# Kernel tuning notes

Measured on AMD Instinct MI355X. Metric: run time of the kernel, lower is better.

Reference implementation:

```python
import jax, jax.numpy as jnp
import numpy as np

N_USER = 100_000
N_ITEM = 100_000
E = 1_600_000
D_IN = 128
H = 64
OUT = 2


def _lin_init(k, din, dout):
    kw, kb = jax.random.split(k)
    bound = 1.0 / np.sqrt(din)
    W = jax.random.uniform(kw, (din, dout), jnp.float32, -bound, bound)
    b = jax.random.uniform(kb, (dout,), jnp.float32, -bound, bound)
    return W, b


def setup_inputs() -> dict:
    key = jax.random.key(0)
    ks = jax.random.split(key, 12)
    inp = {
        "x_user": jax.random.normal(ks[0], (N_USER, D_IN), jnp.float32),
        "x_item": jax.random.normal(ks[1], (N_ITEM, D_IN), jnp.float32),
        "ei_user": jax.random.randint(ks[2], (2, E), 0, N_USER, jnp.int32),
        "ei_item": jax.random.randint(ks[3], (2, E), 0, N_ITEM, jnp.int32),
    }
    inp["W1_user"], inp["b1_user"] = _lin_init(ks[4], D_IN, H)
    inp["W1_item"], inp["b1_item"] = _lin_init(ks[5], D_IN, H)
    inp["W2_user"], inp["b2_user"] = _lin_init(ks[6], H, H)
    inp["W2_item"], inp["b2_item"] = _lin_init(ks[7], H, H)
    inp["Wl_user"], inp["bl_user"] = _lin_init(ks[8], H, OUT)
    inp["Wl_item"], inp["bl_item"] = _lin_init(ks[9], H, OUT)
    return inp


def gcn_conv(x, W, b, src, dst, n):
    # PyG GCNConv: h = x @ W; symmetric norm with added self-loops; scatter-add to dst; + bias
    loop = jnp.arange(n, dtype=src.dtype)
    s = jnp.concatenate([src, loop])  # [E+n]
    d = jnp.concatenate([dst, loop])
    deg = jax.ops.segment_sum(jnp.ones(s.shape[0], x.dtype), d, num_segments=n)
    dinv = jnp.where(deg > 0, jax.lax.rsqrt(deg), 0.0)
    norm = dinv[s] * dinv[d]  # [E+n]
    h = x @ W  # [n, out]
    msg = h[s] * norm[:, None]  # gather + scale, [E+n, out]
    return jax.ops.segment_sum(msg, d, num_segments=n) + b


def reference(x_user, x_item, ei_user, ei_item,
              W1_user, b1_user, W1_item, b1_item,
              W2_user, b2_user, W2_item, b2_item,
              Wl_user, bl_user, Wl_item, bl_item):
    # layer 1 (HeteroConv with one GCNConv per node type's relation) + relu; dropout = identity (eval)
    h_u = jax.nn.relu(gcn_conv(x_user, W1_user, b1_user, ei_user[0], ei_user[1], N_USER))
    h_i = jax.nn.relu(gcn_conv(x_item, W1_item, b1_item, ei_item[0], ei_item[1], N_ITEM))
    # layer 2 + relu
    h_u = jax.nn.relu(gcn_conv(h_u, W2_user, b2_user, ei_user[0], ei_user[1], N_USER))
    h_i = jax.nn.relu(gcn_conv(h_i, W2_item, b2_item, ei_item[0], ei_item[1], N_ITEM))
    # per-node-type output heads
    return (h_u @ Wl_user + bl_user, h_i @ Wl_item + bl_item)
```

## Files before the change

### kernel.cpp

```cpp
#include <hip/hip_runtime.h>

#define CDIV(a,b) (((a)+(b)-1)/(b))
#define NPB 256
#define PCHUNK 2048

typedef __attribute__((ext_vector_type(8))) short bf16x8;
typedef __attribute__((ext_vector_type(8))) unsigned short u16x8;
typedef __attribute__((ext_vector_type(4))) float f32x4;

__device__ __forceinline__ unsigned short f2bf(float x){
    unsigned int u = __float_as_uint(x);
    unsigned int r = u + 0x7FFFu + ((u >> 16) & 1u);
    return (unsigned short)(r >> 16);
}
__device__ __forceinline__ float bf2f(unsigned short h){
    return __uint_as_float(((unsigned int)h) << 16);
}

__global__ __launch_bounds__(256) void hg_wsplit_all(const float* __restrict__ W1u, const float* __restrict__ W1i,
                                                     const float* __restrict__ W2u, const float* __restrict__ W2i,
                                                     unsigned short* __restrict__ Bhi, unsigned short* __restrict__ Blo){
    const int sid = blockIdx.x*256 + threadIdx.x;
    if (sid >= 3072) return;
    const float* W; int slot, base;
    if (sid < 1024)      { W = W1u; slot = sid;        base = 0;     }
    else if (sid < 2048) { W = W1i; slot = sid - 1024; base = 8192;  }
    else if (sid < 2560) { W = W2u; slot = sid - 2048; base = 16384; }
    else                 { W = W2i; slot = sid - 2560; base = 20480; }
    const int l  = slot & 63;
    const int ct = (slot >> 6) & 3;
    const int ks = slot >> 8;
    const int kb = ks*32 + (l >> 4)*8;
    const int c  = ct*16 + (l & 15);
    #pragma unroll
    for (int j = 0; j < 8; ++j){
        const float w = W[(size_t)(kb + j)*64 + c];
        const unsigned short h = f2bf(w);
        Bhi[(size_t)base + (size_t)slot*8 + j] = h;
        Blo[(size_t)base + (size_t)slot*8 + j] = f2bf(w - bf2f(h));
    }
}

__device__ __forceinline__ void gemm1_body(int gb,
                                           const float* __restrict__ XU, const float* __restrict__ XI,
                                           const unsigned short* __restrict__ Bhi, const unsigned short* __restrict__ Blo,
                                           unsigned short* __restrict__ GU, unsigned short* __restrict__ GI,
                                           int NU, int NI, int gbU){
    const int type = (gb >= gbU);
    const int blk  = type ? gb - gbU : gb;
    const float* X = type ? XI : XU;
    unsigned short* G = type ? GI : GU;
    const int N    = type ? NI : NU;
    const unsigned short* Bh = Bhi + (type ? 8192 : 0);
    const unsigned short* Bl = Blo + (type ? 8192 : 0);

    const int l = threadIdx.x & 63;
    const int w = threadIdx.x >> 6;
    const int row0 = blk*64 + w*16;
    if (row0 >= N) return;

    f32x4 acc[4];
    #pragma unroll
    for (int ct = 0; ct < 4; ++ct) acc[ct] = (f32x4){0.f,0.f,0.f,0.f};

    const int rA = row0 + (l & 15);
    const int kg = (l >> 4) * 8;
    const bool rowok = (rA < N);
    const float* xrow = X + (size_t)rA * 128;

    #pragma unroll
    for (int ks = 0; ks < 4; ++ks){
        float xv[8];
        if (rowok){
            const float4 a = *(const float4*)(xrow + ks*32 + kg);
            const float4 b = *(const float4*)(xrow + ks*32 + kg + 4);
            xv[0]=a.x; xv[1]=a.y; xv[2]=a.z; xv[3]=a.w;
            xv[4]=b.x; xv[5]=b.y; xv[6]=b.z; xv[7]=b.w;
        } else {
            #pragma unroll
            for (int j = 0; j < 8; ++j) xv[j] = 0.f;
        }
        bf16x8 ahi, alo;
        #pragma unroll
        for (int j = 0; j < 8; ++j){
            const unsigned short h = f2bf(xv[j]);
            ahi[j] = (short)h;
            alo[j] = (short)f2bf(xv[j] - bf2f(h));
        }
        #pragma unroll
        for (int ct = 0; ct < 4; ++ct){
            const bf16x8 bhi = *(const bf16x8*)(Bh + ((size_t)(ks*4 + ct)*64 + l)*8);
            const bf16x8 blo = *(const bf16x8*)(Bl + ((size_t)(ks*4 + ct)*64 + l)*8);
            acc[ct] = __builtin_amdgcn_mfma_f32_16x16x32_bf16(ahi, bhi, acc[ct], 0, 0, 0);
            acc[ct] = __builtin_amdgcn_mfma_f32_16x16x32_bf16(alo, bhi, acc[ct], 0, 0, 0);
            acc[ct] = __builtin_amdgcn_mfma_f32_16x16x32_bf16(ahi, blo, acc[ct], 0, 0, 0);
        }
    }

    const int orow0 = row0 + (l >> 4)*4;
    const int ocol  = l & 15;
    #pragma unroll
    for (int r = 0; r < 4; ++r){
        const int orow = orow0 + r;
        if (orow < N){
            #pragma unroll
            for (int ct = 0; ct < 4; ++ct)
                G[(size_t)orow*64 + ct*16 + ocol] = f2bf(acc[ct][r]);
        }
    }
}

#define GEMM_TAIL(taskTot) \
    if ((int)blockIdx.x >= (taskTot)){ \
        gemm1_body(goff + blockIdx.x - (taskTot), XU, XI, Bhi, Blo, GU, GI, NU, NI, gbU); \
        return; \
    }

__global__ __launch_bounds__(256) void hg_mega_chist(const int* __restrict__ eiU, const int* __restrict__ eiI,
                                                     int* __restrict__ chU, int* __restrict__ chI,
                                                     int EU, int EI, int pbU, int pbTot, int NB,
                                                     const float* __restrict__ XU, const float* __restrict__ XI,
                                                     const unsigned short* __restrict__ Bhi, const unsigned short* __restrict__ Blo,
                                                     unsigned short* __restrict__ GU, unsigned short* __restrict__ GI,
                                                     int NU, int NI, int gbU, int goff){
    GEMM_TAIL(pbTot)
    extern __shared__ int sh[];
    const int type = ((int)blockIdx.x >= pbU);
    const int blk  = type ? blockIdx.x - pbU : blockIdx.x;
    const int E    = type ? EI : EU;
    const int* dst = (type ? eiI : eiU) + E;
    int* chist     = (type ? chI : chU) + (size_t)blk * NB;
    for (int i = threadIdx.x; i < NB; i += 256) sh[i] = 0;
    __syncthreads();
    const int e0 = blk * PCHUNK;
    const int eend = min(e0 + PCHUNK, E);
    for (int e = e0 + threadIdx.x; e < eend; e += 256)
        atomicAdd(&sh[dst[e] >> 8], 1);
    __syncthreads();
    for (int i = threadIdx.x; i < NB; i += 256)
        chist[i] = sh[i];
}

__global__ __launch_bounds__(256) void hg_mega_colscan(int* __restrict__ chU, int* __restrict__ chI,
                                                       int* __restrict__ bhU, int* __restrict__ bhI,
                                                       int pbU, int pbI, int NB,
                                                       const float* __restrict__ XU, const float* __restrict__ XI,
                                                       const unsigned short* __restrict__ Bhi, const unsigned short* __restrict__ Blo,
                                                       unsigned short* __restrict__ GU, unsigned short* __restrict__ GI,
                                                       int NU, int NI, int gbU, int goff){
    GEMM_TAIL(2*NB)
    __shared__ int sc[256];
    const int type = ((int)blockIdx.x >= NB);
    const int b    = type ? blockIdx.x - NB : blockIdx.x;
    int* chist     = type ? chI : chU;
    int* bh        = type ? bhI : bhU;
    const int nch  = type ? pbI : pbU;
    const int t = threadIdx.x;
    int carry = 0;
    for (int seg = 0; seg < nch; seg += 256){
        const int idx = seg + t;
        const int v = (idx < nch) ? chist[(size_t)idx*NB + b] : 0;
        sc[t] = v;
        __syncthreads();
        for (int off = 1; off < 256; off <<= 1){
            int x = 0;
            if (t >= off) x = sc[t-off];
            __syncthreads();
            if (t >= off) sc[t] += x;
            __syncthreads();
        }
        if (idx < nch) chist[(size_t)idx*NB + b] = carry + sc[t] - v;
        const int tot = sc[255];
        __syncthreads();
        carry += tot;
    }
    if (t == 0) bh[b] = carry;
}

__global__ __launch_bounds__(256) void hg_mega_bscan(const int* __restrict__ bhU, const int* __restrict__ bhI,
                                                     int* __restrict__ boffU, int* __restrict__ boffI,
                                                     int NB, int EU, int EI,
                                                     const float* __restrict__ XU, const float* __restrict__ XI,
                                                     const unsigned short* __restrict__ Bhi, const unsigned short* __restrict__ Blo,
                                                     unsigned short* __restrict__ GU, unsigned short* __restrict__ GI,
                                                     int NU, int NI, int gbU, int goff){
    GEMM_TAIL(2)
    __shared__ int sc[256];
    const int type = blockIdx.x;
    const int* bh = type ? bhI : bhU;
    int* boff     = type ? boffI : boffU;
    const int E   = type ? EI : EU;
    const int t = threadIdx.x;
    const int i0 = 2*t, i1 = 2*t + 1;
    const int c0 = (i0 < NB) ? bh[i0] : 0;
    const int c1 = (i1 < NB) ? bh[i1] : 0;
    const int s = c0 + c1;
    sc[t] = s;
    __syncthreads();
    for (int off = 1; off < 256; off <<= 1){
        int x = 0;
        if (t >= off) x = sc[t-off];
        __syncthreads();
        if (t >= off) sc[t] += x;
        __syncthreads();
    }
    const int excl = sc[t] - s;
    if (i0 < NB) boff[i0] = excl;
    if (i1 < NB) boff[i1] = excl + c0;
    if (t == 0) boff[NB] = E;
}

__global__ __launch_bounds__(256) void hg_mega_part(const int* __restrict__ eiU, const int* __restrict__ eiI,
                                                    const int* __restrict__ chU, const int* __restrict__ chI,
                                                    const int* __restrict__ boffU, const int* __restrict__ boffI,
                                                    unsigned int* __restrict__ bkU, unsigned int* __restrict__ bkI,
                                                    int EU, int EI, int pbU, int pbTot, int NB,
                                                    const float* __restrict__ XU, const float* __restrict__ XI,
                                                    const unsigned short* __restrict__ Bhi, const unsigned short* __restrict__ Blo,
                                                    unsigned short* __restrict__ GU, unsigned short* __restrict__ GI,
                                                    int NU, int NI, int gbU, int goff){
    GEMM_TAIL(pbTot)
    extern __shared__ int sh[];
    int* lofs  = sh;
    int* lcur  = lofs + NB;
    int* lbase = lcur + NB;
    int* sc    = lbase + NB;
    unsigned int* stage = (unsigned int*)(sc + 256);
    int* gaddr = (int*)(stage + PCHUNK);

    const int type = ((int)blockIdx.x >= pbU);
    const int blk  = type ? blockIdx.x - pbU : blockIdx.x;
    const int E    = type ? EI : EU;
    const int* src = type ? eiI : eiU;
    const int* dst = src + E;
    const int* chist = (type ? chI : chU) + (size_t)blk * NB;
    const int* boff  = type ? boffI : boffU;
    unsigned int* bucketed = type ? bkI : bkU;

    const int t  = threadIdx.x;
    const int e0 = blk * PCHUNK;
    const int eend = min(e0 + PCHUNK, E);
    const int cnt  = eend - e0;

    int se[8], de[8];
    for (int i = t; i < NB; i += 256) lofs[i] = 0;
    __syncthreads();
    const int eb = e0 + t*8;
    if (eb + 8 <= E){
        const int4 sa = *(const int4*)(src + eb);
        const int4 sb = *(const int4*)(src + eb + 4);
        const int4 da = *(const int4*)(dst + eb);
        const int4 db = *(const int4*)(dst + eb + 4);
        se[0]=sa.x; se[1]=sa.y; se[2]=sa.z; se[3]=sa.w;
        se[4]=sb.x; se[5]=sb.y; se[6]=sb.z; se[7]=sb.w;
        de[0]=da.x; de[1]=da.y; de[2]=da.z; de[3]=da.w;
        de[4]=db.x; de[5]=db.y; de[6]=db.z; de[7]=db.w;
    } else {
        #pragma unroll
        for (int j = 0; j < 8; ++j){
            const int e = eb + j;
            se[j] = (e < E) ? src[e] : -1;
            de[j] = (e < E) ? dst[e] : -1;
        }
    }
    #pragma unroll
    for (int j = 0; j < 8; ++j)
        if (de[j] >= 0) atomicAdd(&lofs[de[j] >> 8], 1);
    __syncthreads();

    const int i0 = 2*t, i1 = 2*t + 1;
    const int c0 = (i0 < NB) ? lofs[i0] : 0;
    const int c1 = (i1 < NB) ? lofs[i1] : 0;
    if (i0 < NB) lbase[i0] = boff[i0] + chist[i0];
    if (i1 < NB) lbase[i1] = boff[i1] + chist[i1];
    const int s = c0 + c1;
    sc[t] = s;
    __syncthreads();
    for (int off = 1; off < 256; off <<= 1){
        int x = 0;
        if (t >= off) x = sc[t-off];
        __syncthreads();
        if (t >= off) sc[t] += x;
        __syncthreads();
    }
    const int excl = sc[t] - s;
    __syncthreads();
    if (i0 < NB){ lofs[i0] = excl;      lcur[i0] = excl; }
    if (i1 < NB){ lofs[i1] = excl + c0; lcur[i1] = excl + c0; }
    __syncthreads();

    #pragma unroll
    for (int j = 0; j < 8; ++j){
        if (de[j] >= 0){
            const int b = de[j] >> 8;
            const int p = atomicAdd(&lcur[b], 1);
            stage[p] = (unsigned int)se[j] | ((unsigned int)(de[j] & 255) << 24);
            gaddr[p] = lbase[b] + (p - lofs[b]);
        }
    }
    __syncthreads();

    for (int i = t; i < cnt; i += 256)
        bucketed[gaddr[i]] = stage[i];
}

__global__ __launch_bounds__(256) void hg_mega_build(const unsigned int* __restrict__ bkU, const unsigned int* __restrict__ bkI,
                                                     const int* __restrict__ boffU, const int* __restrict__ boffI,
                                                     float* __restrict__ dinvU, float* __restrict__ dinvI,
                                                     int* __restrict__ rowptrU, int* __restrict__ rowptrI,
                                                     int* __restrict__ csrU, int* __restrict__ csrI,
                                                     int NU, int NI, int EU, int EI, int nbU, int nbTot,
                                                     const float* __restrict__ XU, const float* __restrict__ XI,
                                                     const unsigned short* __restrict__ Bhi, const unsigned short* __restrict__ Blo,
                                                     unsigned short* __restrict__ GU, unsigned short* __restrict__ GI,
                                                     int gbU, int goff){
    GEMM_TAIL(nbTot)
    __shared__ int hist[NPB];
    __shared__ int sc[NPB];
    __shared__ int cur[NPB];
    const int type = ((int)blockIdx.x >= nbU);
    const int b    = type ? blockIdx.x - nbU : blockIdx.x;
    const unsigned int* bucketed = type ? bkI : bkU;
    const int* boff = type ? boffI : boffU;
    float* dinv     = type ? dinvI : dinvU;
    int* rowptr     = type ? rowptrI : rowptrU;
    int* csr_src    = type ? csrI : csrU;
    const int N     = type ? NI : NU;
    const int E     = type ? EI : EU;

    const int t   = threadIdx.x;
    const int beg = boff[b], end = boff[b+1];
    hist[t] = 0;
    __syncthreads();
    for (int i = beg + t; i < end; i += 256)
        atomicAdd(&hist[bucketed[i] >> 24], 1);
    __syncthreads();
    const int d = hist[t];
    sc[t] = d;
    __syncthreads();
    for (int off = 1; off < 256; off <<= 1){
        int x = 0;
        if (t >= off) x = sc[t-off];
        __syncthreads();
        if (t >= off) sc[t] += x;
        __syncthreads();
    }
    const int excl = sc[t] - d;
    const int v = b*NPB + t;
    if (v < N){
        dinv[v]   = rsqrtf((float)(d + 1));
        rowptr[v] = beg + excl;
    }
    if (b == 0 && t == 0) rowptr[N] = E;
    cur[t] = beg + excl;
    __syncthreads();
    for (int i = beg + t; i < end; i += 256){
        const unsigned int w = bucketed[i];
        const int p = atomicAdd(&cur[w >> 24], 1);
        csr_src[p] = (int)(w & 0x00FFFFFFu);
    }
}

__device__ __forceinline__ void gather_core(const unsigned short* __restrict__ g,
                                            const int* __restrict__ csr_src, const int* __restrict__ rowptr,
                                            const float* __restrict__ dinv, int v, int c8, bool ok,
                                            float* acc, float& dvv){
    int beg = 0, cnt = 0;
    dvv = 0.f;
    if (ok){ beg = rowptr[v]; cnt = rowptr[v+1] - beg; dvv = dinv[v]; }

    #pragma unroll
    for (int j = 0; j < 8; ++j) acc[j] = 0.f;
    if (ok){
        const u16x8 s = *(const u16x8*)(g + (size_t)v*64 + c8);
        #pragma unroll
        for (int j = 0; j < 8; ++j) acc[j] = bf2f(s[j]) * dvv;
    }

    int i = 0;
    for (; i + 8 <= cnt; i += 8){
        const int s0 = csr_src[beg+i+0]; const int s1 = csr_src[beg+i+1];
        const int s2 = csr_src[beg+i+2]; const int s3 = csr_src[beg+i+3];
        const int s4 = csr_src[beg+i+4]; const int s5 = csr_src[beg+i+5];
        const int s6 = csr_src[beg+i+6]; const int s7 = csr_src[beg+i+7];
        const float dv0 = dinv[s0]; const float dv1 = dinv[s1];
        const float dv2 = dinv[s2]; const float dv3 = dinv[s3];
        const float dv4 = dinv[s4]; const float dv5 = dinv[s5];
        const float dv6 = dinv[s6]; const float dv7 = dinv[s7];
        const u16x8 x0 = *(const u16x8*)(g + (size_t)s0*64 + c8);
        const u16x8 x1 = *(const u16x8*)(g + (size_t)s1*64 + c8);
        const u16x8 x2 = *(const u16x8*)(g + (size_t)s2*64 + c8);
        const u16x8 x3 = *(const u16x8*)(g + (size_t)s3*64 + c8);
        const u16x8 x4 = *(const u16x8*)(g + (size_t)s4*64 + c8);
        const u16x8 x5 = *(const u16x8*)(g + (size_t)s5*64 + c8);
        const u16x8 x6 = *(const u16x8*)(g + (size_t)s6*64 + c8);
        const u16x8 x7 = *(const u16x8*)(g + (size_t)s7*64 + c8);
        #pragma unroll
        for (int j = 0; j < 8; ++j){
            float a = fmaf(bf2f(x0[j]), dv0, fmaf(bf2f(x1[j]), dv1, fmaf(bf2f(x2[j]), dv2, bf2f(x3[j]) * dv3)));
            float c = fmaf(bf2f(x4[j]), dv4, fmaf(bf2f(x5[j]), dv5, fmaf(bf2f(x6[j]), dv6, bf2f(x7[j]) * dv7)));
            acc[j] += a + c;
        }
    }
    for (; i + 4 <= cnt; i += 4){
        const int s0 = csr_src[beg+i+0]; const int s1 = csr_src[beg+i+1];
        const int s2 = csr_src[beg+i+2]; const int s3 = csr_src[beg+i+3];
        const float dv0 = dinv[s0]; const float dv1 = dinv[s1];
        const float dv2 = dinv[s2]; const float dv3 = dinv[s3];
        const u16x8 x0 = *(const u16x8*)(g + (size_t)s0*64 + c8);
        const u16x8 x1 = *(const u16x8*)(g + (size_t)s1*64 + c8);
        const u16x8 x2 = *(const u16x8*)(g + (size_t)s2*64 + c8);
        const u16x8 x3 = *(const u16x8*)(g + (size_t)s3*64 + c8);
        #pragma unroll
        for (int j = 0; j < 8; ++j)
            acc[j] += fmaf(bf2f(x0[j]), dv0, fmaf(bf2f(x1[j]), dv1, fmaf(bf2f(x2[j]), dv2, bf2f(x3[j]) * dv3)));
    }
    for (; i < cnt; ++i){
        const int s0 = csr_src[beg+i];
        const float dv0 = dinv[s0];
        const u16x8 x0 = *(const u16x8*)(g + (size_t)s0*64 + c8);
        #pragma unroll
        for (int j = 0; j < 8; ++j) acc[j] = fmaf(bf2f(x0[j]), dv0, acc[j]);
    }
}

__global__ __launch_bounds__(256) void hg_agg_gemm2(const unsigned short* __restrict__ gU, const unsigned short* __restrict__ gI,
                                                    const int* __restrict__ csrU, const int* __restrict__ csrI,
                                                    const int* __restrict__ rowptrU, const int* __restrict__ rowptrI,
                                                    const float* __restrict__ dinvU, const float* __restrict__ dinvI,
                                                    const float* __restrict__ bU, const float* __restrict__ bI,
                                                    const unsigned short* __restrict__ Bhi, const unsigned short* __restrict__ Blo,
                                                    unsigned short* __restrict__ G2U, unsigned short* __restrict__ G2I,
                                                    int NU, int NI, int nbU){
    __shared__ float hrow[32*68];
    const int type = ((int)blockIdx.x >= nbU);
    const int blk  = type ? blockIdx.x - nbU : blockIdx.x;
    const unsigned short* g = type ? gI : gU;
    const int* csr_src = type ? csrI : csrU;
    const int* rowptr  = type ? rowptrI : rowptrU;
    const float* dinv  = type ? dinvI : dinvU;
    const float* b     = type ? bI : bU;
    unsigned short* G2 = type ? G2I : G2U;
    const int N        = type ? NI : NU;
    const unsigned short* Bh = Bhi + (type ? 20480 : 16384);
    const unsigned short* Bl = Blo + (type ? 20480 : 16384);

    const int t = threadIdx.x;
    const int nodeLocal = t >> 3;
    const int c8 = (t & 7) << 3;
    const int v = blk*32 + nodeLocal;
    const bool ok = (v < N);

    float acc[8]; float dvv;
    gather_core(g, csr_src, rowptr, dinv, v, c8, ok, acc, dvv);

    {
        const float4 b0 = *(const float4*)(b + c8);
        const float4 b1 = *(const float4*)(b + c8 + 4);
        float r0 = ok ? fmaxf(fmaf(acc[0], dvv, b0.x), 0.f) : 0.f;
        float r1 = ok ? fmaxf(fmaf(acc[1], dvv, b0.y), 0.f) : 0.f;
        float r2 = ok ? fmaxf(fmaf(acc[2], dvv, b0.z), 0.f) : 0.f;
        float r3 = ok ? fmaxf(fmaf(acc[3], dvv, b0.w), 0.f) : 0.f;
        float r4 = ok ? fmaxf(fmaf(acc[4], dvv, b1.x), 0.f) : 0.f;
        float r5 = ok ? fmaxf(fmaf(acc[5], dvv, b1.y), 0.f) : 0.f;
        float r6 = ok ? fmaxf(fmaf(acc[6], dvv, b1.z), 0.f) : 0.f;
        float r7 = ok ? fmaxf(fmaf(acc[7], dvv, b1.w), 0.f) : 0.f;
        float* hr = hrow + nodeLocal*68 + c8;
        hr[0]=r0; hr[1]=r1; hr[2]=r2; hr[3]=r3; hr[4]=r4; hr[5]=r5; hr[6]=r6; hr[7]=r7;
    }
    __syncthreads();

    const int l  = t & 63;
    const int wv = t >> 6;
    const int rbase  = (wv & 1) * 16;
    const int ctbase = (wv >> 1) * 2;

    f32x4 acc2[2];
    acc2[0] = (f32x4){0.f,0.f,0.f,0.f};
    acc2[1] = (f32x4){0.f,0.f,0.f,0.f};

    const int arow = rbase + (l & 15);
    const int kg   = (l >> 4) * 8;
    #pragma unroll
    for (int ks = 0; ks < 2; ++ks){
        const float* hr = hrow + arow*68 + ks*32 + kg;
        const float4 a = *(const float4*)(hr);
        const float4 c = *(const float4*)(hr + 4);
        float xv[8] = {a.x,a.y,a.z,a.w,c.x,c.y,c.z,c.w};
        bf16x8 ahi, alo;
        #pragma unroll
        for (int j = 0; j < 8; ++j){
            const unsigned short h = f2bf(xv[j]);
            ahi[j] = (short)h;
            alo[j] = (short)f2bf(xv[j] - bf2f(h));
        }
        #pragma unroll
        for (int ct = 0; ct < 2; ++ct){
            const int slot = (ks*4 + ctbase + ct)*64 + l;
            const bf16x8 bhi = *(const bf16x8*)(Bh + (size_t)slot*8);
            const bf16x8 blo = *(const bf16x8*)(Bl + (size_t)slot*8);
            acc2[ct] = __builtin_amdgcn_mfma_f32_16x16x32_bf16(ahi, bhi, acc2[ct], 0, 0, 0);
            acc2[ct] = __builtin_amdgcn_mfma_f32_16x16x32_bf16(alo, bhi, acc2[ct], 0, 0, 0);
            acc2[ct] = __builtin_amdgcn_mfma_f32_16x16x32_bf16(ahi, blo, acc2[ct], 0, 0, 0);
        }
    }

    const int orow0 = rbase + (l >> 4)*4;
    const int ocol  = l & 15;
    #pragma unroll
    for (int r = 0; r < 4; ++r){
        const int gv = blk*32 + orow0 + r;
        if (gv < N){
            #pragma unroll
            for (int ct = 0; ct < 2; ++ct)
                G2[(size_t)gv*64 + (ctbase + ct)*16 + ocol] = f2bf(acc2[ct][r]);
        }
    }
}

__global__ __launch_bounds__(256) void hg_agghead(const unsigned short* __restrict__ gU, const unsigned short* __restrict__ gI,
                                                  const int* __restrict__ csrU, const int* __restrict__ csrI,
                                                  const int* __restrict__ rowptrU, const int* __restrict__ rowptrI,
                                                  const float* __restrict__ dinvU, const float* __restrict__ dinvI,
                                                  const float* __restrict__ bU, const float* __restrict__ bI,
                                                  const float* __restrict__ WlU, const float* __restrict__ WlI,
                                                  const float* __restrict__ blU, const float* __restrict__ blI,
                                                  float* __restrict__ outU, float* __restrict__ outI,
                                                  int NU, int NI, int nbU){
    const int type = ((int)blockIdx.x >= nbU);
    const int blk  = type ? blockIdx.x - nbU : blockIdx.x;
    const unsigned short* g = type ? gI : gU;
    const int* csr_src = type ? csrI : csrU;
    const int* rowptr  = type ? rowptrI : rowptrU;
    const float* dinv  = type ? dinvI : dinvU;
    const float* b     = type ? bI : bU;
    const float* Wl    = type ? WlI : WlU;
    const float* bl    = type ? blI : blU;
    float* outp        = type ? outI : outU;
    const int N        = type ? NI : NU;

    const int t = threadIdx.x;
    const int nodeLocal = t >> 3;
    const int c8 = (t & 7) << 3;
    const int v = blk*32 + nodeLocal;
    const bool ok = (v < N);

    float acc[8]; float dvv;
    gather_core(g, csr_src, rowptr, dinv, v, c8, ok, acc, dvv);

    float r[8];
    {
        const float4 b0 = *(const float4*)(b + c8);
        const float4 b1 = *(const float4*)(b + c8 + 4);
        r[0] = fmaxf(fmaf(acc[0], dvv, b0.x), 0.f);
        r[1] = fmaxf(fmaf(acc[1], dvv, b0.y), 0.f);
        r[2] = fmaxf(fmaf(acc[2], dvv, b0.z), 0.f);
        r[3] = fmaxf(fmaf(acc[3], dvv, b0.w), 0.f);
        r[4] = fmaxf(fmaf(acc[4], dvv, b1.x), 0.f);
        r[5] = fmaxf(fmaf(acc[5], dvv, b1.y), 0.f);
        r[6] = fmaxf(fmaf(acc[6], dvv, b1.z), 0.f);
        r[7] = fmaxf(fmaf(acc[7], dvv, b1.w), 0.f);
    }

    float p0 = 0.f, p1 = 0.f;
    #pragma unroll
    for (int j = 0; j < 8; ++j){
        const float2 wl = *(const float2*)(Wl + (size_t)(c8 + j)*2);
        p0 = fmaf(r[j], wl.x, p0);
        p1 = fmaf(r[j], wl.y, p1);
    }
    p0 += __shfl_xor(p0, 1); p1 += __shfl_xor(p1, 1);
    p0 += __shfl_xor(p0, 2); p1 += __shfl_xor(p1, 2);
    p0 += __shfl_xor(p0, 4); p1 += __shfl_xor(p1, 4);
    if (ok && (t & 7) == 0){
        float2 o; o.x = p0 + bl[0]; o.y = p1 + bl[1];
        *(float2*)(outp + (size_t)v*2) = o;
    }
}

extern "C" void kernel_launch(void* const* d_in, const int* in_sizes, int n_in,
                              void* d_out, int out_size, void* d_ws, size_t ws_size,
                              hipStream_t stream) {
    const float* x_user = (const float*)d_in[0];
    const float* x_item = (const float*)d_in[1];
    const int*  ei_user = (const int*)d_in[2];
    const int*  ei_item = (const int*)d_in[3];
    const float* W1_user = (const float*)d_in[4];
    const float* b1_user = (const float*)d_in[5];
    const float* W1_item = (const float*)d_in[6];
    const float* b1_item = (const float*)d_in[7];
    const float* W2_user = (const float*)d_in[8];
    const float* b2_user = (const float*)d_in[9];
    const float* W2_item = (const float*)d_in[10];
    const float* b2_item = (const float*)d_in[11];
    const float* Wl_user = (const float*)d_in[12];
    const float* bl_user = (const float*)d_in[13];
    const float* Wl_item = (const float*)d_in[14];
    const float* bl_item = (const float*)d_in[15];

    const int NU = in_sizes[0] / 128;
    const int NI = in_sizes[1] / 128;
    const int EU = in_sizes[2] / 2;
    const int EI = in_sizes[3] / 2;
    const int NBU = CDIV(NU, NPB);
    const int NBI = CDIV(NI, NPB);
    const int NB  = (NBU > NBI) ? NBU : NBI;
    const int pbU = CDIV(EU, PCHUNK), pbI = CDIV(EI, PCHUNK);

    char* w = (char*)d_ws;
    unsigned short* GU = (unsigned short*)w;    w += (size_t)NU * 64 * sizeof(unsigned short);
    unsigned short* GI = (unsigned short*)w;    w += (size_t)NI * 64 * sizeof(unsigned short);
    unsigned short* G2U = (unsigned short*)w;   w += (size_t)NU * 64 * sizeof(unsigned short);
    unsigned short* G2I = (unsigned short*)w;   w += (size_t)NI * 64 * sizeof(unsigned short);
    float* dinvU = (float*)w;                   w += (size_t)NU * sizeof(float);
    float* dinvI = (float*)w;                   w += (size_t)NI * sizeof(float);
    int* rowptrU = (int*)w;                     w += ((size_t)NU + 1) * sizeof(int);
    int* rowptrI = (int*)w;                     w += ((size_t)NI + 1) * sizeof(int);
    int* csrU = (int*)w;                        w += (size_t)EU * sizeof(int);
    int* csrI = (int*)w;                        w += (size_t)EI * sizeof(int);
    unsigned int* bkU = (unsigned int*)w;       w += (size_t)EU * sizeof(int);
    unsigned int* bkI = (unsigned int*)w;       w += (size_t)EI * sizeof(int);
    int* chU = (int*)w;                         w += (size_t)pbU * NB * sizeof(int);
    int* chI = (int*)w;                         w += (size_t)pbI * NB * sizeof(int);
    int* bhU = (int*)w;                         w += (size_t)NB * sizeof(int);
    int* bhI = (int*)w;                         w += (size_t)NB * sizeof(int);
    int* boffU = (int*)w;                       w += ((size_t)NB + 1) * sizeof(int);
    int* boffI = (int*)w;                       w += ((size_t)NB + 1) * sizeof(int);
    unsigned short* Bhi = (unsigned short*)w;   w += (size_t)24576 * sizeof(unsigned short);
    unsigned short* Blo = (unsigned short*)w;   w += (size_t)24576 * sizeof(unsigned short);

    float* out  = (float*)d_out;
    float* outU = out;
    float* outI = out + (size_t)2 * NU;

    const int gbU = CDIV(NU, 64), gbI = CDIV(NI, 64);
    const int GB = gbU + gbI;
    const int q = GB / 5;
    const int c1 = q, c2 = q, c3 = q, c4 = q, c5 = GB - 4*q;

    hg_wsplit_all<<<12, 256, 0, stream>>>(W1_user, W1_item, W2_user, W2_item, Bhi, Blo);

    hg_mega_chist<<<pbU + pbI + c1, 256, NB*sizeof(int), stream>>>(
        ei_user, ei_item, chU, chI, EU, EI, pbU, pbU + pbI, NB,
        x_user, x_item, Bhi, Blo, GU, GI, NU, NI, gbU, 0);
    hg_mega_colscan<<<2*NB + c2, 256, 0, stream>>>(
        chU, chI, bhU, bhI, pbU, pbI, NB,
        x_user, x_item, Bhi, Blo, GU, GI, NU, NI, gbU, c1);
    hg_mega_bscan<<<2 + c3, 256, 0, stream>>>(
        bhU, bhI, boffU, boffI, NB, EU, EI,
        x_user, x_item, Bhi, Blo, GU, GI, NU, NI, gbU, c1 + c2);
    const size_t p5lds = (size_t)(3*NB + 256 + 2*PCHUNK) * sizeof(int);
    hg_mega_part<<<pbU + pbI + c4, 256, p5lds, stream>>>(
        ei_user, ei_item, chU, chI, boffU, boffI, bkU, bkI, EU, EI, pbU, pbU + pbI, NB,
        x_user, x_item, Bhi, Blo, GU, GI, NU, NI, gbU, c1 + c2 + c3);
    hg_mega_build<<<NBU + NBI + c5, 256, 0, stream>>>(
        bkU, bkI, boffU, boffI, dinvU, dinvI, rowptrU, rowptrI, csrU, csrI,
        NU, NI, EU, EI, NBU, NBU + NBI,
        x_user, x_item, Bhi, Blo, GU, GI, gbU, c1 + c2 + c3 + c4);

    const int abU = CDIV(NU, 32), abI = CDIV(NI, 32);
    hg_agg_gemm2<<<abU + abI, 256, 0, stream>>>(GU, GI, csrU, csrI, rowptrU, rowptrI,
                                                dinvU, dinvI, b1_user, b1_item,
                                                Bhi, Blo, G2U, G2I, NU, NI, abU);

    hg_agghead<<<abU + abI, 256, 0, stream>>>(G2U, G2I, csrU, csrI, rowptrU, rowptrI,
                                              dinvU, dinvI, b2_user, b2_item,
                                              Wl_user, Wl_item, bl_user, bl_item,
                                              outU, outI, NU, NI, abU);
}
```

Baseline: 240.7 us.

## Merge weight split into histogram kernel and fold bucket scan via last-block

Cuts the preprocessing chain from six launches to four. The weight bf16 hi/lo split now runs as extra blocks of the histogram kernel. The bucket-offset scan is done by whichever column-scan block finishes last, detected with an atomic counter and threadfence. The layer-1 GEMM tail blocks are spread over three kernels instead of five, and the weight split no longer overlaps with the GEMM because it now shares a kernel with the histogram. The last-block pattern leaves one block doing a serial tail scan, and it relies on the counter being reset inside the first kernel.

```diff
diff --git a/kernel.cpp b/kernel.cpp
--- a/kernel.cpp
+++ b/kernel.cpp
@@ -3,6 +3,7 @@
 #define CDIV(a,b) (((a)+(b)-1)/(b))
 #define NPB 256
 #define PCHUNK 2048
+#define WSB 12
 
 typedef __attribute__((ext_vector_type(8))) short bf16x8;
 typedef __attribute__((ext_vector_type(8))) unsigned short u16x8;
@@ -15,30 +16,6 @@
 }
 __device__ __forceinline__ float bf2f(unsigned short h){
     return __uint_as_float(((unsigned int)h) << 16);
-}
-
-__global__ __launch_bounds__(256) void hg_wsplit_all(const float* __restrict__ W1u, const float* __restrict__ W1i,
-                                                     const float* __restrict__ W2u, const float* __restrict__ W2i,
-                                                     unsigned short* __restrict__ Bhi, unsigned short* __restrict__ Blo){
-    const int sid = blockIdx.x*256 + threadIdx.x;
-    if (sid >= 3072) return;
-    const float* W; int slot, base;
-    if (sid < 1024)      { W = W1u; slot = sid;        base = 0;     }
-    else if (sid < 2048) { W = W1i; slot = sid - 1024; base = 8192;  }
-    else if (sid < 2560) { W = W2u; slot = sid - 2048; base = 16384; }
-    else                 { W = W2i; slot = sid - 2560; base = 20480; }
-    const int l  = slot & 63;
-    const int ct = (slot >> 6) & 3;
-    const int ks = slot >> 8;
-    const int kb = ks*32 + (l >> 4)*8;
-    const int c  = ct*16 + (l & 15);
-    #pragma unroll
-    for (int j = 0; j < 8; ++j){
-        const float w = W[(size_t)(kb + j)*64 + c];
-        const unsigned short h = f2bf(w);
-        Bhi[(size_t)base + (size_t)slot*8 + j] = h;
-        Blo[(size_t)base + (size_t)slot*8 + j] = f2bf(w - bf2f(h));
-    }
 }
 
 __device__ __forceinline__ void gemm1_body(int gb,
@@ -116,17 +93,39 @@
         return; \
     }
 
-__global__ __launch_bounds__(256) void hg_mega_chist(const int* __restrict__ eiU, const int* __restrict__ eiI,
-                                                     int* __restrict__ chU, int* __restrict__ chI,
-                                                     int EU, int EI, int pbU, int pbTot, int NB,
-                                                     const float* __restrict__ XU, const float* __restrict__ XI,
-                                                     const unsigned short* __restrict__ Bhi, const unsigned short* __restrict__ Blo,
-                                                     unsigned short* __restrict__ GU, unsigned short* __restrict__ GI,
-                                                     int NU, int NI, int gbU, int goff){
-    GEMM_TAIL(pbTot)
+__global__ __launch_bounds__(256) void hg_link1(const float* __restrict__ W1u, const float* __restrict__ W1i,
+                                                const float* __restrict__ W2u, const float* __restrict__ W2i,
+                                                unsigned short* __restrict__ Bhi, unsigned short* __restrict__ Blo,
+                                                const int* __restrict__ eiU, const int* __restrict__ eiI,
+                                                int* __restrict__ chU, int* __restrict__ chI,
+                                                int EU, int EI, int pbU, int NB, int* __restrict__ done){
+    if (blockIdx.x == 0 && threadIdx.x == 0) *done = 0;
+    if ((int)blockIdx.x < WSB){
+        const int sid = blockIdx.x*256 + threadIdx.x;
+        if (sid >= 3072) return;
+        const float* W; int slot, base;
+        if (sid < 1024)      { W = W1u; slot = sid;        base = 0;     }
+        else if (sid < 2048) { W = W1i; slot = sid - 1024; base = 8192;  }
+        else if (sid < 2560) { W = W2u; slot = sid - 2048; base = 16384; }
+        else                 { W = W2i; slot = sid - 2560; base = 20480; }
+        const int l  = slot & 63;
+        const int ct = (slot >> 6) & 3;
+        const int ks = slot >> 8;
+        const int kb = ks*32 + (l >> 4)*8;
+        const int c  = ct*16 + (l & 15);
+        #pragma unroll
+        for (int j = 0; j < 8; ++j){
+            const float w = W[(size_t)(kb + j)*64 + c];
+            const unsigned short h = f2bf(w);
+            Bhi[(size_t)base + (size_t)slot*8 + j] = h;
+            Blo[(size_t)base + (size_t)slot*8 + j] = f2bf(w - bf2f(h));
+        }
+        return;
+    }
     extern __shared__ int sh[];
-    const int type = ((int)blockIdx.x >= pbU);
-    const int blk  = type ? blockIdx.x - pbU : blockIdx.x;
+    const int cb   = blockIdx.x - WSB;
+    const int type = (cb >= pbU);
+    const int blk  = type ? cb - pbU : cb;
     const int E    = type ? EI : EU;
     const int* dst = (type ? eiI : eiU) + E;
     int* chist     = (type ? chI : chU) + (size_t)blk * NB;
@@ -141,15 +140,18 @@
         chist[i] = sh[i];
 }
 
-__global__ __launch_bounds__(256) void hg_mega_colscan(int* __restrict__ chU, int* __restrict__ chI,
-                                                       int* __restrict__ bhU, int* __restrict__ bhI,
-                                                       int pbU, int pbI, int NB,
-                                                       const float* __restrict__ XU, const float* __restrict__ XI,
-                                                       const unsigned short* __restrict__ Bhi, const unsigned short* __restrict__ Blo,
-                                                       unsigned short* __restrict__ GU, unsigned short* __restrict__ GI,
-                                                       int NU, int NI, int gbU, int goff){
+__global__ __launch_bounds__(256) void hg_link2(int* __restrict__ chU, int* __restrict__ chI,
+                                                int* __restrict__ bhU, int* __restrict__ bhI,
+                                                int* __restrict__ boffU, int* __restrict__ boffI,
+                                                int pbU, int pbI, int NB, int EU, int EI,
+                                                int* __restrict__ done,
+                                                const float* __restrict__ XU, const float* __restrict__ XI,
+                                                const unsigned short* __restrict__ Bhi, const unsigned short* __restrict__ Blo,
+                                                unsigned short* __restrict__ GU, unsigned short* __restrict__ GI,
+                                                int NU, int NI, int gbU, int goff){
     GEMM_TAIL(2*NB)
     __shared__ int sc[256];
+    __shared__ int winner;
     const int type = ((int)blockIdx.x >= NB);
     const int b    = type ? blockIdx.x - NB : blockIdx.x;
     int* chist     = type ? chI : chU;
@@ -175,50 +177,48 @@
         carry += tot;
     }
     if (t == 0) bh[b] = carry;
-}
-
-__global__ __launch_bounds__(256) void hg_mega_bscan(const int* __restrict__ bhU, const int* __restrict__ bhI,
-                                                     int* __restrict__ boffU, int* __restrict__ boffI,
-                                                     int NB, int EU, int EI,
-                                                     const float* __restrict__ XU, const float* __restrict__ XI,
-                                                     const unsigned short* __restrict__ Bhi, const unsigned short* __restrict__ Blo,
-                                                     unsigned short* __restrict__ GU, unsigned short* __restrict__ GI,
-                                                     int NU, int NI, int gbU, int goff){
-    GEMM_TAIL(2)
-    __shared__ int sc[256];
-    const int type = blockIdx.x;
-    const int* bh = type ? bhI : bhU;
-    int* boff     = type ? boffI : boffU;
-    const int E   = type ? EI : EU;
-    const int t = threadIdx.x;
-    const int i0 = 2*t, i1 = 2*t + 1;
-    const int c0 = (i0 < NB) ? bh[i0] : 0;
-    const int c1 = (i1 < NB) ? bh[i1] : 0;
-    const int s = c0 + c1;
-    sc[t] = s;
-    __syncthreads();
-    for (int off = 1; off < 256; off <<= 1){
-        int x = 0;
-        if (t >= off) x = sc[t-off];
-        __syncthreads();
-        if (t >= off) sc[t] += x;
-        __syncthreads();
-    }
-    const int excl = sc[t] - s;
-    if (i0 < NB) boff[i0] = excl;
-    if (i1 < NB) boff[i1] = excl + c0;
-    if (t == 0) boff[NB] = E;
-}
-
-__global__ __launch_bounds__(256) void hg_mega_part(const int* __restrict__ eiU, const int* __restrict__ eiI,
-                                                    const int* __restrict__ chU, const int* __restrict__ chI,
-                                                    const int* __restrict__ boffU, const int* __restrict__ boffI,
-                                                    unsigned int* __restrict__ bkU, unsigned int* __restrict__ bkI,
-                                                    int EU, int EI, int pbU, int pbTot, int NB,
-                                                    const float* __restrict__ XU, const float* __restrict__ XI,
-                                                    const unsigned short* __restrict__ Bhi, const unsigned short* __restrict__ Blo,
-                                                    unsigned short* __restrict__ GU, unsigned short* __restrict__ GI,
-                                                    int NU, int NI, int gbU, int goff){
+    __threadfence();
+    if (t == 0){
+        const int old = atomicAdd(done, 1);
+        winner = (old == 2*NB - 1);
+    }
+    __syncthreads();
+    if (!winner) return;
+    __threadfence();
+    for (int ty = 0; ty < 2; ++ty){
+        const int* bhp = ty ? bhI : bhU;
+        int* boff      = ty ? boffI : boffU;
+        const int E    = ty ? EI : EU;
+        const int i0 = 2*t, i1 = 2*t + 1;
+        const int c0 = (i0 < NB) ? bhp[i0] : 0;
+        const int c1 = (i1 < NB) ? bhp[i1] : 0;
+        const int s = c0 + c1;
+        sc[t] = s;
+        __syncthreads();
+        for (int off = 1; off < 256; off <<= 1){
+            int x = 0;
+            if (t >= off) x = sc[t-off];
+            __syncthreads();
+            if (t >= off) sc[t] += x;
+            __syncthreads();
+        }
+        const int excl = sc[t] - s;
+        if (i0 < NB) boff[i0] = excl;
+        if (i1 < NB) boff[i1] = excl + c0;
+        if (t == 0) boff[NB] = E;
+        __syncthreads();
+    }
+}
+
+__global__ __launch_bounds__(256) void hg_link3(const int* __restrict__ eiU, const int* __restrict__ eiI,
+                                                const int* __restrict__ chU, const int* __restrict__ chI,
+                                                const int* __restrict__ boffU, const int* __restrict__ boffI,
+                                                unsigned int* __restrict__ bkU, unsigned int* __restrict__ bkI,
+                                                int EU, int EI, int pbU, int pbTot, int NB,
+                                                const float* __restrict__ XU, const float* __restrict__ XI,
+                                                const unsigned short* __restrict__ Bhi, const unsigned short* __restrict__ Blo,
+                                                unsigned short* __restrict__ GU, unsigned short* __restrict__ GI,
+                                                int NU, int NI, int gbU, int goff){
     GEMM_TAIL(pbTot)
     extern __shared__ int sh[];
     int* lofs  = sh;
@@ -304,16 +304,16 @@
         bucketed[gaddr[i]] = stage[i];
 }
 
-__global__ __launch_bounds__(256) void hg_mega_build(const unsigned int* __restrict__ bkU, const unsigned int* __restrict__ bkI,
-                                                     const int* __restrict__ boffU, const int* __restrict__ boffI,
-                                                     float* __restrict__ dinvU, float* __restrict__ dinvI,
-                                                     int* __restrict__ rowptrU, int* __restrict__ rowptrI,
-                                                     int* __restrict__ csrU, int* __restrict__ csrI,
-                                                     int NU, int NI, int EU, int EI, int nbU, int nbTot,
-                                                     const float* __restrict__ XU, const float* __restrict__ XI,
-                                                     const unsigned short* __restrict__ Bhi, const unsigned short* __restrict__ Blo,
-                                                     unsigned short* __restrict__ GU, unsigned short* __restrict__ GI,
-                                                     int gbU, int goff){
+__global__ __launch_bounds__(256) void hg_link4(const unsigned int* __restrict__ bkU, const unsigned int* __restrict__ bkI,
+                                                const int* __restrict__ boffU, const int* __restrict__ boffI,
+                                                float* __restrict__ dinvU, float* __restrict__ dinvI,
+                                                int* __restrict__ rowptrU, int* __restrict__ rowptrI,
+                                                int* __restrict__ csrU, int* __restrict__ csrI,
+                                                int NU, int NI, int EU, int EI, int nbU, int nbTot,
+                                                const float* __restrict__ XU, const float* __restrict__ XI,
+                                                const unsigned short* __restrict__ Bhi, const unsigned short* __restrict__ Blo,
+                                                unsigned short* __restrict__ GU, unsigned short* __restrict__ GI,
+                                                int gbU, int goff){
     GEMM_TAIL(nbTot)
     __shared__ int hist[NPB];
     __shared__ int sc[NPB];
@@ -626,6 +626,7 @@
     int* bhI = (int*)w;                         w += (size_t)NB * sizeof(int);
     int* boffU = (int*)w;                       w += ((size_t)NB + 1) * sizeof(int);
     int* boffI = (int*)w;                       w += ((size_t)NB + 1) * sizeof(int);
+    int* done  = (int*)w;                       w += sizeof(int);
     unsigned short* Bhi = (unsigned short*)w;   w += (size_t)24576 * sizeof(unsigned short);
     unsigned short* Blo = (unsigned short*)w;   w += (size_t)24576 * sizeof(unsigned short);
 
@@ -635,28 +636,26 @@
 
     const int gbU = CDIV(NU, 64), gbI = CDIV(NI, 64);
     const int GB = gbU + gbI;
-    const int q = GB / 5;
-    const int c1 = q, c2 = q, c3 = q, c4 = q, c5 = GB - 4*q;
-
-    hg_wsplit_all<<<12, 256, 0, stream>>>(W1_user, W1_item, W2_user, W2_item, Bhi, Blo);
-
-    hg_mega_chist<<<pbU + pbI + c1, 256, NB*sizeof(int), stream>>>(
-        ei_user, ei_item, chU, chI, EU, EI, pbU, pbU + pbI, NB,
+    const int q = GB / 3;
+    const int c2 = q, c3 = q, c4 = GB - 2*q;
+
+    hg_link1<<<WSB + pbU + pbI, 256, NB*sizeof(int), stream>>>(
+        W1_user, W1_item, W2_user, W2_item, Bhi, Blo,
+        ei_user, ei_item, chU, chI, EU, EI, pbU, NB, done);
+
+    hg_link2<<<2*NB + c2, 256, 0, stream>>>(
+        chU, chI, bhU, bhI, boffU, boffI, pbU, pbI, NB, EU, EI, done,
         x_user, x_item, Bhi, Blo, GU, GI, NU, NI, gbU, 0);
-    hg_mega_colscan<<<2*NB + c2, 256, 0, stream>>>(
-        chU, chI, bhU, bhI, pbU, pbI, NB,
-        x_user, x_item, Bhi, Blo, GU, GI, NU, NI, gbU, c1);
-    hg_mega_bscan<<<2 + c3, 256, 0, stream>>>(
-        bhU, bhI, boffU, boffI, NB, EU, EI,
-        x_user, x_item, Bhi, Blo, GU, GI, NU, NI, gbU, c1 + c2);
+
     const size_t p5lds = (size_t)(3*NB + 256 + 2*PCHUNK) * sizeof(int);
-    hg_mega_part<<<pbU + pbI + c4, 256, p5lds, stream>>>(
+    hg_link3<<<pbU + pbI + c3, 256, p5lds, stream>>>(
         ei_user, ei_item, chU, chI, boffU, boffI, bkU, bkI, EU, EI, pbU, pbU + pbI, NB,
-        x_user, x_item, Bhi, Blo, GU, GI, NU, NI, gbU, c1 + c2 + c3);
-    hg_mega_build<<<NBU + NBI + c5, 256, 0, stream>>>(
+        x_user, x_item, Bhi, Blo, GU, GI, NU, NI, gbU, c2);
+
+    hg_link4<<<NBU + NBI + c4, 256, 0, stream>>>(
         bkU, bkI, boffU, boffI, dinvU, dinvI, rowptrU, rowptrI, csrU, csrI,
         NU, NI, EU, EI, NBU, NBU + NBI,
-        x_user, x_item, Bhi, Blo, GU, GI, gbU, c1 + c2 + c3 + c4);
+        x_user, x_item, Bhi, Blo, GU, GI, gbU, c2 + c3);
 
     const int abU = CDIV(NU, 32), abI = CDIV(NI, 32);
     hg_agg_gemm2<<<abU + abI, 256, 0, stream>>>(GU, GI, csrU, csrI, rowptrU, rowptrI,
```

Measured after the change: 312.9 us. 1.3x slower.
